# Kernel tuning notes

Measured on AMD Instinct MI355X. Metric: run time of the kernel, lower is better.

The kernel has to match this reference:

```python
import jax, jax.numpy as jnp
import numpy as np

THRESHOLD = 0.0  # default float threshold, non-learned path
SURROGATE_TAU = 0.1

@jax.custom_vjp
def jumprelu(x):
    # Forward: hard threshold x * 1[x > THRESHOLD]
    return x * (x > THRESHOLD).astype(x.dtype)

def _jumprelu_fwd(x):
    return jumprelu(x), x

def _jumprelu_bwd(x, g):
    # Smooth surrogate gradient of x * sigmoid(x/tau)
    tau = SURROGATE_TAU
    sig = jax.nn.sigmoid(x / tau)
    surrogate = sig + x * sig * (1.0 - sig) / tau
    return (g * surrogate,)

jumprelu.defvjp(_jumprelu_fwd, _jumprelu_bwd)

NUM_TRANSFORMS = 64
D_MODEL = 2048
RANK = 32
BATCH = 2048

def setup_inputs() -> dict:
    key = jax.random.key(0)
    kx, kv, ku, ke = jax.random.split(key, 4)
    scale = (1.0 / (D_MODEL * RANK)) ** 0.25
    x = jax.random.normal(kx, (BATCH, D_MODEL), dtype=jnp.float32)
    V = jax.random.normal(kv, (NUM_TRANSFORMS, RANK, D_MODEL), dtype=jnp.float32) * scale
    U = jax.random.normal(ku, (NUM_TRANSFORMS, D_MODEL, RANK), dtype=jnp.float32) * scale
    encoder = jax.random.normal(ke, (NUM_TRANSFORMS, D_MODEL), dtype=jnp.float32)
    encoder = encoder / jnp.linalg.norm(encoder, axis=1, keepdims=True)
    bias = jnp.full((NUM_TRANSFORMS,), -1.0, dtype=jnp.float32)
    return {"x": x, "V": V, "U": U, "encoder": encoder, "bias": bias}

def reference(x, V, U, encoder, bias):
    # pre_acts: (batch, num_transforms)
    pre_acts = x @ encoder.T - bias
    gate = jumprelu(pre_acts)
    # Vx: (n, b, r); UVx: (n, b, d)
    Vx = jnp.einsum('nrd,bd->nbr', V, x)
    UVx = jnp.einsum('ndr,nbr->nbd', U, Vx)
    gated = UVx * gate.T[:, :, None]
    output = gated.sum(axis=0)  # (batch, d_model)
    u_norms = jnp.linalg.norm(U.reshape(U.shape[0], -1), axis=1)
    v_norms = jnp.linalg.norm(V.reshape(V.shape[0], -1), axis=1)
    frobenius_norms = u_norms * v_norms / (D_MODEL * RANK) ** 0.5
    return (output, gate, frobenius_norms)
```

## Files before the change

kernel.cpp:

```cpp
#include <hip/hip_runtime.h>


#define D_MODEL 2048
#define BATCH   2048
#define NT      64
#define RANK    32

typedef __attribute__((ext_vector_type(8))) __bf16 bf16x8;
typedef __attribute__((ext_vector_type(4))) float  f32x4;

__device__ __forceinline__ unsigned short f2bf(float f) {
  unsigned int u = __builtin_bit_cast(unsigned int, f);
  u += 0x7FFFu + ((u >> 16) & 1u);
  return (unsigned short)(u >> 16);
}

__device__ __forceinline__ void gload_lds16(const void* g, void* l) {
  __builtin_amdgcn_global_load_lds(
      (const __attribute__((address_space(1))) unsigned int*)g,
      (__attribute__((address_space(3))) unsigned int*)l,
      16, 0, 0);
}


__device__ __forceinline__ void block_reduce_store(float ss, float* dst, int slot) {
  __shared__ float red[256];
  int t = threadIdx.x;
  red[t] = ss;
  __syncthreads();
  for (int s = 128; s > 0; s >>= 1) {
    if (t < s) red[t] += red[t + s];
    __syncthreads();
  }
  if (t == 0) dst[slot] = red[0];
}

__global__ void k_prep(const float4* __restrict__ x, const float4* __restrict__ enc,
                       const float4* __restrict__ V, const float4* __restrict__ U,
                       ushort4* __restrict__ xb, ushort4* __restrict__ encb,
                       ushort4* __restrict__ Vb, unsigned short* __restrict__ Ut,
                       float* __restrict__ partV, float* __restrict__ partU) {
  int bid = blockIdx.x, t = threadIdx.x;
  if (bid < 1024) {
#pragma unroll
    for (int it = 0; it < 4; ++it) {
      int i = bid * 1024 + it * 256 + t;
      float4 v = x[i];
      ushort4 o;
      o.x = f2bf(v.x); o.y = f2bf(v.y); o.z = f2bf(v.z); o.w = f2bf(v.w);
      xb[i] = o;
    }
  } else if (bid < 1152) {
    int i = (bid - 1024) * 256 + t;
    float4 v = enc[i];
    ushort4 o;
    o.x = f2bf(v.x); o.y = f2bf(v.y); o.z = f2bf(v.z); o.w = f2bf(v.w);
    encb[i] = o;
  } else if (bid < 1408) {
    int b = bid - 1152;
    size_t base4 = (size_t)b * 4096;
    float ss = 0.f;
    for (int it = 0; it < 16; ++it) {
      size_t idx = base4 + t + it * 256;
      float4 v = V[idx];
      ss += v.x * v.x + v.y * v.y + v.z * v.z + v.w * v.w;
      ushort4 o;
      o.x = f2bf(v.x); o.y = f2bf(v.y); o.z = f2bf(v.z); o.w = f2bf(v.w);
      Vb[idx] = o;
    }
    block_reduce_store(ss, partV, b);
  } else {
    int b = bid - 1408;
    int n = b >> 2;
    size_t base4 = (size_t)b * 4096;
    float ss = 0.f;
    for (int it = 0; it < 16; ++it) {
      size_t idx4 = base4 + t + it * 256;
      float4 v = U[idx4];
      ss += v.x * v.x + v.y * v.y + v.z * v.z + v.w * v.w;
      size_t e = idx4 * 4 - (size_t)n * (D_MODEL * RANK);
      int dcol = (int)(e >> 5);
      int r = (int)(e & 31);
      ushort4 o;
      o.x = f2bf(v.x); o.y = f2bf(v.y); o.z = f2bf(v.z); o.w = f2bf(v.w);
      *(ushort4*)(Ut + (size_t)dcol * 2048 + n * 32 + r) = o;
    }
    block_reduce_store(ss, partU, b);
  }
}

__global__ void k_gate_reduce(const float* __restrict__ part, const float* __restrict__ bias,
                              float* __restrict__ gate,
                              const float* __restrict__ pU, const float* __restrict__ pV,
                              float* __restrict__ frob) {
  int t = threadIdx.x;
  if (blockIdx.x == 0 && t < NT) {
    float su = pU[4 * t] + pU[4 * t + 1] + pU[4 * t + 2] + pU[4 * t + 3];
    float sv = pV[4 * t] + pV[4 * t + 1] + pV[4 * t + 2] + pV[4 * t + 3];
    frob[t] = sqrtf(su) * sqrtf(sv) * (1.0f / 256.0f);
  }
#pragma unroll
  for (int u = 0; u < 4; ++u) {
    int idx = blockIdx.x * 1024 + u * 256 + t;
    float s = 0.f;
#pragma unroll
    for (int z = 0; z < 8; ++z) s += part[(size_t)z * (BATCH * NT) + idx];
    float pre = s - bias[idx & (NT - 1)];
    gate[idx] = pre > 0.f ? pre : 0.f;
  }
}

template <int WGM, int WGN, int MI, int NJ, int EPI, int SWZ>
__global__ void gemm_bt(const unsigned short* __restrict__ A,
                        const unsigned short* __restrict__ Bt,
                        const float* __restrict__ aux,
                        unsigned short* __restrict__ outB,
                        float* __restrict__ outF, int K, int klen) {
  constexpr int BM = WGM * MI * 16;
  constexpr int BN = WGN * NJ * 16;
  constexpr int RA = BM / 32;
  constexpr int RB = BN / 32;
  __shared__ __align__(16) unsigned short smem[(BM + BN) * 64];
  unsigned short* As = smem;
  unsigned short* Bs = smem + BM * 64;

  const int tid = threadIdx.x;
  const int w = tid >> 6;
  const int lane = tid & 63;
  const int quad = lane >> 4;
  const int l15 = lane & 15;
  const int wm = w % WGM;
  const int wn = w / WGM;

  int blockM, blockN, kbeg;
  if constexpr (SWZ) {
    const int lin = blockIdx.x;
    const int xcd = lin & 7;
    const int i = lin >> 3;
    blockM = (xcd & 1) * 8 + (i & 7);
    blockN = (xcd >> 1) * 8 + (i >> 3);
    kbeg = 0;
  } else {
    blockN = blockIdx.x;
    blockM = blockIdx.y;
    kbeg = blockIdx.z * klen;
  }

  const int lrow = lane >> 3;
  const int lq = (lane & 7) ^ lrow;
  const unsigned short* Ag = A + (size_t)(blockM * BM + lrow) * K + kbeg + lq * 8;
  const unsigned short* Bg = Bt + (size_t)(blockN * BN + lrow) * K + kbeg + lq * 8;

  const int pcs = (quad ^ (lane & 7)) * 16;
  const int rfA = wm * MI * 16 + l15;
  const int rfB = wn * NJ * 16 + l15;

  f32x4 acc[MI][NJ];
  const f32x4 z = {0.f, 0.f, 0.f, 0.f};
#pragma unroll
  for (int i = 0; i < MI; ++i)
#pragma unroll
    for (int j = 0; j < NJ; ++j) acc[i][j] = z;

  for (int k0 = 0; k0 < klen; k0 += 64) {
#pragma unroll
    for (int j = 0; j < RA; ++j)
      gload_lds16(Ag + (size_t)((j * 4 + w) * 8) * K + k0,
                  (char*)As + (j * 4 + w) * 1024);
#pragma unroll
    for (int j = 0; j < RB; ++j)
      gload_lds16(Bg + (size_t)((j * 4 + w) * 8) * K + k0,
                  (char*)Bs + (j * 4 + w) * 1024);
    __syncthreads();
#pragma unroll
    for (int s = 0; s < 2; ++s) {
      bf16x8 af[MI], bfr[NJ];
#pragma unroll
      for (int i = 0; i < MI; ++i)
        af[i] = *(const bf16x8*)((const char*)As + (rfA + i * 16) * 128 + (pcs ^ (s << 6)));
#pragma unroll
      for (int j = 0; j < NJ; ++j)
        bfr[j] = *(const bf16x8*)((const char*)Bs + (rfB + j * 16) * 128 + (pcs ^ (s << 6)));
#pragma unroll
      for (int i = 0; i < MI; ++i)
#pragma unroll
        for (int j = 0; j < NJ; ++j)
          acc[i][j] = __builtin_amdgcn_mfma_f32_16x16x32_bf16(af[i], bfr[j], acc[i][j], 0, 0, 0);
    }
    __syncthreads();
  }

  const int row0 = blockM * BM + wm * MI * 16 + quad * 4;
  const int col0 = blockN * BN + wn * NJ * 16 + l15;
#pragma unroll
  for (int i = 0; i < MI; ++i) {
#pragma unroll
    for (int j = 0; j < NJ; ++j) {
      const int col = col0 + j * 16;
#pragma unroll
      for (int t = 0; t < 4; ++t) {
        const int row = row0 + i * 16 + t;
        float v = acc[i][j][t];
        if constexpr (EPI == 0) {
          float g = aux[(size_t)row * NT + (col >> 5)];
          outB[(size_t)row * 2048 + col] = f2bf(v * g);
        } else if constexpr (EPI == 1) {
          outF[(size_t)row * 2048 + col] = v;
        } else {
          outF[(size_t)blockIdx.z * (BATCH * NT) + (size_t)row * NT + col] = v;
        }
      }
    }
  }
}


extern "C" void kernel_launch(void* const* d_in, const int* in_sizes, int n_in,
                              void* d_out, int out_size, void* d_ws, size_t ws_size,
                              hipStream_t stream) {
  const float* x    = (const float*)d_in[0];
  const float* V    = (const float*)d_in[1];
  const float* U    = (const float*)d_in[2];
  const float* enc  = (const float*)d_in[3];
  const float* bias = (const float*)d_in[4];

  float* out  = (float*)d_out;
  float* gate = out + (size_t)BATCH * D_MODEL;
  float* frob = gate + (size_t)BATCH * NT;

  char* ws = (char*)d_ws;
  unsigned short* xb   = (unsigned short*)(ws);
  unsigned short* Vb   = (unsigned short*)(ws + (8u << 20));
  unsigned short* Ut   = (unsigned short*)(ws + (16u << 20));
  unsigned short* Yg   = (unsigned short*)(ws + (24u << 20));
  float* gatePart      = (float*)Yg;
  unsigned short* encb = (unsigned short*)(ws + (32u << 20));
  float* partU = (float*)(ws + (32u << 20) + 262144);
  float* partV = partU + 256;

  k_prep<<<1664, 256, 0, stream>>>((const float4*)x, (const float4*)enc,
                                   (const float4*)V, (const float4*)U,
                                   (ushort4*)xb, (ushort4*)encb, (ushort4*)Vb, Ut,
                                   partV, partU);

  gemm_bt<4, 1, 2, 4, 3, 0><<<dim3(1, 16, 8), 256, 0, stream>>>(
      xb, encb, nullptr, nullptr, gatePart, D_MODEL, 256);
  k_gate_reduce<<<128, 256, 0, stream>>>(gatePart, bias, gate, partU, partV, frob);

  gemm_bt<2, 2, 4, 2, 0, 1><<<512, 256, 0, stream>>>(
      xb, Vb, gate, Yg, nullptr, D_MODEL, D_MODEL);

  gemm_bt<2, 2, 4, 2, 1, 1><<<512, 256, 0, stream>>>(
      Yg, Ut, nullptr, nullptr, out, D_MODEL, D_MODEL);
}
```

Measured before the change: 166.4 us.

## Split K across two warp teams per block with LDS reduction in big GEMMs

New measurement: 154.1 us. -7.4%, faster.

```diff
diff --git a/kernel.cpp b/kernel.cpp
--- a/kernel.cpp
+++ b/kernel.cpp
@@ -110,27 +110,31 @@
   }
 }
 
-template <int WGM, int WGN, int MI, int NJ, int EPI, int SWZ>
-__global__ void gemm_bt(const unsigned short* __restrict__ A,
-                        const unsigned short* __restrict__ Bt,
-                        const float* __restrict__ aux,
-                        unsigned short* __restrict__ outB,
-                        float* __restrict__ outF, int K, int klen) {
+template <int WGM, int WGN, int MI, int NJ, int EPI, int SWZ, int TEAMS>
+__global__ __launch_bounds__(TEAMS * 256, 4)
+void gemm_bt(const unsigned short* __restrict__ A,
+             const unsigned short* __restrict__ Bt,
+             const float* __restrict__ aux,
+             unsigned short* __restrict__ outB,
+             float* __restrict__ outF, int K, int klen) {
   constexpr int BM = WGM * MI * 16;
   constexpr int BN = WGN * NJ * 16;
   constexpr int RA = BM / 32;
   constexpr int RB = BN / 32;
-  __shared__ __align__(16) unsigned short smem[(BM + BN) * 64];
-  unsigned short* As = smem;
-  unsigned short* Bs = smem + BM * 64;
+  __shared__ __align__(16) unsigned short smem[TEAMS * (BM + BN) * 64];
 
   const int tid = threadIdx.x;
   const int w = tid >> 6;
   const int lane = tid & 63;
   const int quad = lane >> 4;
   const int l15 = lane & 15;
-  const int wm = w % WGM;
-  const int wn = w / WGM;
+  const int team = w >> 2;
+  const int wl = w & 3;
+  const int wm = wl % WGM;
+  const int wn = wl / WGM;
+
+  unsigned short* As = smem + team * (BM + BN) * 64;
+  unsigned short* Bs = As + BM * 64;
 
   int blockM, blockN, kbeg;
   if constexpr (SWZ) {
@@ -145,6 +149,8 @@
     blockM = blockIdx.y;
     kbeg = blockIdx.z * klen;
   }
+  const int kspan = klen / TEAMS;
+  kbeg += team * kspan;
 
   const int lrow = lane >> 3;
   const int lq = (lane & 7) ^ lrow;
@@ -162,15 +168,15 @@
 #pragma unroll
     for (int j = 0; j < NJ; ++j) acc[i][j] = z;
 
-  for (int k0 = 0; k0 < klen; k0 += 64) {
+  for (int k0 = 0; k0 < kspan; k0 += 64) {
 #pragma unroll
     for (int j = 0; j < RA; ++j)
-      gload_lds16(Ag + (size_t)((j * 4 + w) * 8) * K + k0,
-                  (char*)As + (j * 4 + w) * 1024);
+      gload_lds16(Ag + (size_t)((j * 4 + wl) * 8) * K + k0,
+                  (char*)As + (j * 4 + wl) * 1024);
 #pragma unroll
     for (int j = 0; j < RB; ++j)
-      gload_lds16(Bg + (size_t)((j * 4 + w) * 8) * K + k0,
-                  (char*)Bs + (j * 4 + w) * 1024);
+      gload_lds16(Bg + (size_t)((j * 4 + wl) * 8) * K + k0,
+                  (char*)Bs + (j * 4 + wl) * 1024);
     __syncthreads();
 #pragma unroll
     for (int s = 0; s < 2; ++s) {
@@ -188,6 +194,29 @@
           acc[i][j] = __builtin_amdgcn_mfma_f32_16x16x32_bf16(af[i], bfr[j], acc[i][j], 0, 0, 0);
     }
     __syncthreads();
+  }
+
+  if constexpr (TEAMS == 2) {
+    float4* red = (float4*)smem;
+    if (team == 1) {
+#pragma unroll
+      for (int i = 0; i < MI; ++i)
+#pragma unroll
+        for (int j = 0; j < NJ; ++j) {
+          float4 v = {acc[i][j][0], acc[i][j][1], acc[i][j][2], acc[i][j][3]};
+          red[((wl * MI + i) * NJ + j) * 64 + lane] = v;
+        }
+    }
+    __syncthreads();
+    if (team == 1) return;
+#pragma unroll
+    for (int i = 0; i < MI; ++i)
+#pragma unroll
+      for (int j = 0; j < NJ; ++j) {
+        float4 r = red[((wl * MI + i) * NJ + j) * 64 + lane];
+        acc[i][j][0] += r.x; acc[i][j][1] += r.y;
+        acc[i][j][2] += r.z; acc[i][j][3] += r.w;
+      }
   }
 
   const int row0 = blockM * BM + wm * MI * 16 + quad * 4;
@@ -243,13 +272,13 @@
                                    (ushort4*)xb, (ushort4*)encb, (ushort4*)Vb, Ut,
                                    partV, partU);
 
-  gemm_bt<4, 1, 2, 4, 3, 0><<<dim3(1, 16, 8), 256, 0, stream>>>(
+  gemm_bt<4, 1, 2, 4, 3, 0, 1><<<dim3(1, 16, 8), 256, 0, stream>>>(
       xb, encb, nullptr, nullptr, gatePart, D_MODEL, 256);
   k_gate_reduce<<<128, 256, 0, stream>>>(gatePart, bias, gate, partU, partV, frob);
 
-  gemm_bt<2, 2, 4, 2, 0, 1><<<512, 256, 0, stream>>>(
+  gemm_bt<2, 2, 4, 2, 0, 1, 2><<<dim3(512, 1, 1), 512, 0, stream>>>(
       xb, Vb, gate, Yg, nullptr, D_MODEL, D_MODEL);
 
-  gemm_bt<2, 2, 4, 2, 1, 1><<<512, 256, 0, stream>>>(
+  gemm_bt<2, 2, 4, 2, 1, 1, 2><<<dim3(512, 1, 1), 512, 0, stream>>>(
       Yg, Ut, nullptr, nullptr, out, D_MODEL, D_MODEL);
 }
```
